# Kernel optimization log

Measured on AMD Instinct MI355X. Metric: run time of the kernel, lower is better.

## Reference

```python
import jax, jax.numpy as jnp
import numpy as np

NUM_HEADS = 16
NUM_COMPRESSED_TOKENS = 16


def _make_merge(metric, r):
    # metric: [b, t, d]; indices are computed under stop_gradient (torch no_grad)
    metric = jax.lax.stop_gradient(metric)
    metric = metric / jnp.linalg.norm(metric, axis=-1, keepdims=True)
    a, b = metric[:, ::2], metric[:, 1::2]          # [b, t/2, d] each
    scores = jnp.einsum('btd,bsd->bts', a, b)       # [b, t/2, t/2], d is small (64)
    node_max = scores.max(axis=-1)                  # [b, t/2]
    node_idx = scores.argmax(axis=-1)               # [b, t/2]
    edge_idx = jnp.argsort(-node_max, axis=-1)      # descending
    unm_idx = edge_idx[:, r:]                       # [b, t/2 - r]
    src_idx = edge_idx[:, :r]                       # [b, r]
    dst_idx = jnp.take_along_axis(node_idx, src_idx, axis=-1)  # [b, r]

    def merge(x):
        # x: [b, t, c] -> [b, t - r, c]
        src, dst = x[:, ::2], x[:, 1::2]
        bb = x.shape[0]
        unm = jnp.take_along_axis(src, unm_idx[..., None], axis=1)
        srcg = jnp.take_along_axis(src, src_idx[..., None], axis=1)
        bidx = jnp.arange(bb)[:, None]
        dst = dst.at[bidx, dst_idx].add(srcg)
        return jnp.concatenate([unm, dst], axis=1)

    return merge


def _merge_wavg(merge, x, size):
    if size is None:
        size = jnp.ones_like(x[..., :1])
    x = merge(x * size)
    size = merge(size)
    return x / size, size


def _merge_tokens(x, target_num_token):
    b, p, c = x.shape
    assert p > target_num_token
    # build merge schedule from static shapes (python ints)
    tmp_p = p
    r_merge_list = []
    while tmp_p != target_num_token:
        if tmp_p - target_num_token <= tmp_p // 2:
            r_merge_list.append(tmp_p - target_num_token)
            break
        else:
            r_merge_list.append(tmp_p // 2)
            tmp_p = tmp_p - tmp_p // 2
    dim = c // NUM_HEADS
    size = None
    for r in r_merge_list:
        p = x.shape[1]
        metric = x.reshape(b, p, NUM_HEADS, dim).mean(axis=2)  # [b, p, dim]
        merge = _make_merge(metric, r)
        x, size = _merge_wavg(merge, x, size)
    return x


def setup_inputs() -> dict:
    key = jax.random.key(0)
    k1, k2, k3 = jax.random.split(key, 3)
    vision_dim, llm_dim = 1024, 4096
    x = jax.random.normal(k1, (32, 576, vision_dim), dtype=jnp.float32)
    W1 = jax.random.normal(k2, (vision_dim, llm_dim), dtype=jnp.float32) * 0.02
    b1 = jnp.zeros((llm_dim,), dtype=jnp.float32)
    W2 = jax.random.normal(k3, (llm_dim, llm_dim), dtype=jnp.float32) * 0.02
    b2 = jnp.zeros((llm_dim,), dtype=jnp.float32)
    return {"x": x, "W1": W1, "b1": b1, "W2": W2, "b2": b2,
            "compress": 1, "local_num_frames": -1}


def reference(x, W1, b1, W2, b2, compress, local_num_frames):
    if compress:
        if local_num_frames != -1:
            num_frames = local_num_frames
            x = x.reshape(x.shape[0], -1, x.shape[-1])
        else:
            num_frames = x.shape[0]
            x = x.reshape(1, -1, x.shape[-1])
        num_tome_tokens = NUM_COMPRESSED_TOKENS * num_frames
    else:
        num_tome_tokens = NUM_COMPRESSED_TOKENS * local_num_frames
    x = _merge_tokens(x, num_tome_tokens)
    # projector: Linear -> GELU(exact) -> Linear
    h = jax.nn.gelu(jnp.einsum('btc,cd->btd', x, W1) + b1, approximate=False)
    out = jnp.einsum('btd,de->bte', h, W2) + b2
    return out
```

## Files before the change

kernel.cpp:

```cpp
#include <hip/hip_runtime.h>
#include <hip/hip_bf16.h>


typedef __attribute__((ext_vector_type(8))) short bf16x8;
typedef __attribute__((ext_vector_type(4))) float f32x4;

__global__ __launch_bounds__(256) void metric_kernel(const float* __restrict__ x,
                                                     float* __restrict__ mnorm, int p)
{
    int row  = blockIdx.x * 4 + (threadIdx.x >> 6);
    int lane = threadIdx.x & 63;
    if (row >= p) return;
    const float* xr = x + (size_t)row * 1024;
    float m = 0.f;
#pragma unroll
    for (int h = 0; h < 16; ++h) m += xr[h * 64 + lane];
    m *= 0.0625f;
    float s = m * m;
#pragma unroll
    for (int off = 32; off > 0; off >>= 1) s += __shfl_xor(s, off, 64);
    mnorm[(size_t)row * 64 + lane] = m / sqrtf(s);
}

__global__ __launch_bounds__(256) void scores_kernel(const float* __restrict__ metric,
                                                     float* __restrict__ pmax,
                                                     int* __restrict__ pidx, int P2)
{
    __shared__ float As[64 * 68];
    __shared__ float Bs[64 * 68];
    const int t = threadIdx.x;
    const int i0 = blockIdx.x * 64, j0 = blockIdx.y * 64;

#pragma unroll
    for (int u = 0; u < 16; ++u) {
        int idx = u * 256 + t;
        int d = idx & 63, i = idx >> 6;
        int gi = i0 + i;
        As[d * 68 + i] = (gi < P2) ? metric[(size_t)(2 * gi) * 64 + d] : 0.f;
        int gj = j0 + i;
        Bs[d * 68 + i] = (gj < P2) ? metric[(size_t)(2 * gj + 1) * 64 + d] : 0.f;
    }
    __syncthreads();

    const int tx = t & 15, ty = t >> 4;
    float acc[4][4];
#pragma unroll
    for (int u = 0; u < 4; ++u)
#pragma unroll
        for (int v = 0; v < 4; ++v) acc[u][v] = 0.f;

    for (int d = 0; d < 64; ++d) {
        float4 av = *reinterpret_cast<const float4*>(&As[d * 68 + ty * 4]);
        float4 bv = *reinterpret_cast<const float4*>(&Bs[d * 68 + tx * 4]);
        float a_[4] = {av.x, av.y, av.z, av.w};
        float b_[4] = {bv.x, bv.y, bv.z, bv.w};
#pragma unroll
        for (int u = 0; u < 4; ++u)
#pragma unroll
            for (int v = 0; v < 4; ++v)
                acc[u][v] = fmaf(a_[u], b_[v], acc[u][v]);
    }

#pragma unroll
    for (int u = 0; u < 4; ++u) {
        float best = -3.0e38f; int bj = 0x7fffffff;
#pragma unroll
        for (int v = 0; v < 4; ++v) {
            int j = j0 + tx * 4 + v;
            if (j < P2 && acc[u][v] > best) { best = acc[u][v]; bj = j; }
        }
#pragma unroll
        for (int off = 1; off < 16; off <<= 1) {
            float ob = __shfl_xor(best, off, 64);
            int   oj = __shfl_xor(bj,   off, 64);
            if (ob > best || (ob == best && oj < bj)) { best = ob; bj = oj; }
        }
        if (tx == 0) {
            int gi = i0 + ty * 4 + u;
            if (gi < P2) {
                pmax[(size_t)blockIdx.y * P2 + gi] = best;
                pidx[(size_t)blockIdx.y * P2 + gi] = bj;
            }
        }
    }
}

__global__ __launch_bounds__(256) void reduce_kernel(const float* __restrict__ pmax,
                                                     const int* __restrict__ pidx,
                                                     float* __restrict__ nmax,
                                                     int* __restrict__ nidx,
                                                     int P2, int JS)
{
    int i = blockIdx.x * 256 + threadIdx.x;
    if (i >= P2) return;
    float best = -3.3e38f; int bj = 0;
    for (int js = 0; js < JS; ++js) {
        float v = pmax[(size_t)js * P2 + i];
        if (v > best) { best = v; bj = pidx[(size_t)js * P2 + i]; }
    }
    nmax[i] = best; nidx[i] = bj;
}

__global__ __launch_bounds__(256) void merge_kernel(const float* __restrict__ x,
                                                    const float* __restrict__ size_in,
                                                    const int* __restrict__ nidx,
                                                    const float* __restrict__ nmax,
                                                    float* __restrict__ xout,
                                                    float* __restrict__ size_out, int P2)
{
    int j = blockIdx.x;
    __shared__ int   list[128];
    __shared__ int   cnt_s;
    __shared__ float ns_s;
    if (threadIdx.x == 0) cnt_s = 0;
    __syncthreads();
    for (int i = threadIdx.x; i < P2; i += 256) {
        if (nidx[i] == j) { int p = atomicAdd(&cnt_s, 1); if (p < 128) list[p] = i; }
    }
    __syncthreads();
    int total = cnt_s;
    bool over = (total > 128);
    if (threadIdx.x == 0) {
        float ns = size_in ? size_in[2 * j + 1] : 1.0f;
        if (!over) {
            for (int u = 1; u < total; ++u) {
                int v = list[u]; float kv = nmax[v]; int w = u - 1;
                while (w >= 0) {
                    int lw = list[w]; float kw = nmax[lw];
                    if (kw < kv || (kw == kv && lw > v)) { list[w + 1] = lw; --w; }
                    else break;
                }
                list[w + 1] = v;
            }
            for (int u = 0; u < total; ++u) ns += size_in ? size_in[2 * list[u]] : 1.0f;
        } else {
            for (int i = 0; i < P2; ++i)
                if (nidx[i] == j) ns += size_in ? size_in[2 * i] : 1.0f;
        }
        ns_s = ns;
        size_out[j] = ns;
    }
    __syncthreads();
    float ns   = ns_s;
    float sodd = size_in ? size_in[2 * j + 1] : 1.0f;
    for (int c = threadIdx.x; c < 1024; c += 256) {
        float acc = x[(size_t)(2 * j + 1) * 1024 + c] * sodd;
        if (!over) {
            for (int u = 0; u < total; ++u) {
                int i2 = list[u];
                float si = size_in ? size_in[2 * i2] : 1.0f;
                acc += x[(size_t)(2 * i2) * 1024 + c] * si;
            }
        } else {
            for (int i2 = 0; i2 < P2; ++i2) {
                if (nidx[i2] == j) {
                    float si = size_in ? size_in[2 * i2] : 1.0f;
                    acc += x[(size_t)(2 * i2) * 1024 + c] * si;
                }
            }
        }
        xout[(size_t)j * 1024 + c] = acc / ns;
    }
}

__global__ __launch_bounds__(512) void rank_kernel(const float* __restrict__ nmax,
                                                   int* __restrict__ edgeidx, int n)
{
    int i = threadIdx.x;
    if (i >= n) return;
    float v = nmax[i];
    int r = 0;
    for (int k = 0; k < n; ++k) {
        float u = nmax[k];
        if (u > v || (u == v && k < i)) ++r;
    }
    edgeidx[r] = i;
}

__global__ __launch_bounds__(256) void unm_kernel(const float* __restrict__ x,
                                                  const float* __restrict__ size_in,
                                                  const int* __restrict__ edgeidx,
                                                  float* __restrict__ xout, int r)
{
    int tb = blockIdx.x;
    int i = edgeidx[r + tb];
    float s = size_in[2 * i];
    for (int c = threadIdx.x; c < 1024; c += 256)
        xout[(size_t)tb * 1024 + c] = (x[(size_t)(2 * i) * 1024 + c] * s) / s;
}

__global__ __launch_bounds__(256) void dst6_kernel(const float* __restrict__ x,
                                                   const float* __restrict__ size_in,
                                                   const int* __restrict__ edgeidx,
                                                   const int* __restrict__ nidx,
                                                   float* __restrict__ xout,
                                                   int r, int out_off)
{
    int j = blockIdx.x;
    __shared__ int   list[64];
    __shared__ int   cnt_s;
    __shared__ float ns_s;
    if (threadIdx.x == 0) {
        int n = 0; float ns = size_in[2 * j + 1];
        for (int m = 0; m < r; ++m) {
            int i2 = edgeidx[m];
            if (nidx[i2] == j) { list[n++] = i2; ns += size_in[2 * i2]; }
        }
        cnt_s = n; ns_s = ns;
    }
    __syncthreads();
    int n = cnt_s; float ns = ns_s;
    float sodd = size_in[2 * j + 1];
    for (int c = threadIdx.x; c < 1024; c += 256) {
        float acc = x[(size_t)(2 * j + 1) * 1024 + c] * sodd;
        for (int u = 0; u < n; ++u) {
            int i2 = list[u];
            acc += x[(size_t)(2 * i2) * 1024 + c] * size_in[2 * i2];
        }
        xout[(size_t)(out_off + j) * 1024 + c] = acc / ns;
    }
}

__global__ __launch_bounds__(256) void castx_kernel(const float* __restrict__ in,
                                                    __hip_bfloat16* __restrict__ out, int n)
{
    int i = blockIdx.x * 256 + threadIdx.x;
    if (i < n) out[i] = __float2bfloat16(in[i]);
}

__global__ __launch_bounds__(256) void transcast_kernel(const float* __restrict__ in,
                                                        __hip_bfloat16* __restrict__ outT,
                                                        int K, int N)
{
    __shared__ float tile[32][33];
    int n0 = blockIdx.x * 32, k0 = blockIdx.y * 32;
    int tx = threadIdx.x & 31, ty = threadIdx.x >> 5;
#pragma unroll
    for (int u = 0; u < 4; ++u) {
        int k = k0 + ty + u * 8;
        tile[ty + u * 8][tx] = in[(size_t)k * N + n0 + tx];
    }
    __syncthreads();
#pragma unroll
    for (int u = 0; u < 4; ++u) {
        int n = n0 + ty + u * 8;
        outT[(size_t)n * K + k0 + tx] = __float2bfloat16(tile[tx][ty + u * 8]);
    }
}

template <int ACT, int OUTBF16>
__global__ __launch_bounds__(256) void mfma_gemm_kernel(
    const unsigned short* __restrict__ A,
    const unsigned short* __restrict__ Bt,
    const float* __restrict__ bias,
    void* __restrict__ Cout, int M, int N, int K)
{
    __shared__ unsigned short As[64 * 64];
    __shared__ unsigned short Bs[64 * 64];
    const int t = threadIdx.x;
    const int lane = t & 63, wave = t >> 6;
    const int wm = wave >> 1, wn = wave & 1;
    const int bi = blockIdx.y * 64, bj = blockIdx.x * 64;
    const int l15 = lane & 15, lg = lane >> 4;

    f32x4 acc[2][2];
#pragma unroll
    for (int m = 0; m < 2; ++m)
#pragma unroll
        for (int n = 0; n < 2; ++n)
#pragma unroll
            for (int r = 0; r < 4; ++r) acc[m][n][r] = 0.f;

    for (int k0 = 0; k0 < K; k0 += 64) {
        __syncthreads();
#pragma unroll
        for (int q = 0; q < 2; ++q) {
            int c = q * 256 + t;
            int row = c >> 3, cc = c & 7;
            int sc = cc ^ (row & 7);
            *reinterpret_cast<int4*>(&As[row * 64 + sc * 8]) =
                *reinterpret_cast<const int4*>(A + (size_t)(bi + row) * K + k0 + cc * 8);
            *reinterpret_cast<int4*>(&Bs[row * 64 + sc * 8]) =
                *reinterpret_cast<const int4*>(Bt + (size_t)(bj + row) * K + k0 + cc * 8);
        }
        __syncthreads();
#pragma unroll
        for (int kc = 0; kc < 2; ++kc) {
            bf16x8 af[2], bfr[2];
#pragma unroll
            for (int m = 0; m < 2; ++m) {
                int row = wm * 32 + m * 16 + l15;
                int c = kc * 4 + lg;
                int sc = c ^ (row & 7);
                af[m] = *reinterpret_cast<const bf16x8*>(&As[row * 64 + sc * 8]);
            }
#pragma unroll
            for (int n = 0; n < 2; ++n) {
                int col = wn * 32 + n * 16 + l15;
                int c = kc * 4 + lg;
                int sc = c ^ (col & 7);
                bfr[n] = *reinterpret_cast<const bf16x8*>(&Bs[col * 64 + sc * 8]);
            }
#pragma unroll
            for (int m = 0; m < 2; ++m)
#pragma unroll
                for (int n = 0; n < 2; ++n)
                    acc[m][n] = __builtin_amdgcn_mfma_f32_16x16x32_bf16(
                        af[m], bfr[n], acc[m][n], 0, 0, 0);
        }
    }

#pragma unroll
    for (int m = 0; m < 2; ++m) {
#pragma unroll
        for (int n = 0; n < 2; ++n) {
            int gcol = bj + wn * 32 + n * 16 + l15;
            float bv = bias[gcol];
#pragma unroll
            for (int r = 0; r < 4; ++r) {
                int grow = bi + wm * 32 + m * 16 + lg * 4 + r;
                float v = acc[m][n][r] + bv;
                if (ACT) v = 0.5f * v * (1.0f + erff(v * 0.70710678118654752440f));
                if (OUTBF16)
                    ((__hip_bfloat16*)Cout)[(size_t)grow * N + gcol] = __float2bfloat16(v);
                else
                    ((float*)Cout)[(size_t)grow * N + gcol] = v;
            }
        }
    }
}

extern "C" void kernel_launch(void* const* d_in, const int* in_sizes, int n_in,
                              void* d_out, int out_size, void* d_ws, size_t ws_size,
                              hipStream_t stream)
{
    const float* x_in = (const float*)d_in[0];
    const float* W1   = (const float*)d_in[1];
    const float* b1   = (const float*)d_in[2];
    const float* W2   = (const float*)d_in[3];
    const float* b2   = (const float*)d_in[4];
    float* out = (float*)d_out;

    const size_t XBYTES = (size_t)9216 * 1024 * 4;
    char* base = (char*)d_ws;
    float* xA     = (float*)base;
    float* xB     = (float*)(base + XBYTES);
    float* metric = (float*)(base + 2 * XBYTES);
    char*  tail   = base + 2 * XBYTES + (size_t)18432 * 64 * 4;
    float* sizeA  = (float*)tail;               tail += 9216 * 4;
    float* sizeB  = (float*)tail;               tail += 9216 * 4;
    float* nmax   = (float*)tail;               tail += 9216 * 4;
    int*   nidx   = (int*)tail;                 tail += 9216 * 4;
    int*   edgeidx= (int*)tail;                 tail += 2048;

    __hip_bfloat16* W2t  = (__hip_bfloat16*)xA;
    __hip_bfloat16* h_bf = (__hip_bfloat16*)((char*)xB + (2u << 20));
    __hip_bfloat16* xbf  = (__hip_bfloat16*)((char*)xB + (6u << 20));
    __hip_bfloat16* W1t  = (__hip_bfloat16*)((char*)xB + (7u << 20));

    const int pcount[6] = {18432, 9216, 4608, 2304, 1152, 576};
    float* xbufs[2] = {xA, xB};
    float* sbufs[2] = {sizeA, sizeB};

    const float* xcur = x_in;
    const float* scur = nullptr;

    for (int rd = 0; rd < 6; ++rd) {
        int p  = pcount[rd];
        int P2 = p / 2;
        float* xout = xbufs[rd & 1];
        float* sout = sbufs[rd & 1];
        float* pmax = xout;
        int*   pidx = (int*)((char*)xout + (16u << 20));

        metric_kernel<<<dim3((p + 3) / 4), dim3(256), 0, stream>>>(xcur, metric, p);

        int JB = (P2 + 63) / 64;
        scores_kernel<<<dim3(JB, JB), dim3(256), 0, stream>>>(metric, pmax, pidx, P2);
        reduce_kernel<<<dim3((P2 + 255) / 256), dim3(256), 0, stream>>>(
            pmax, pidx, nmax, nidx, P2, JB);

        if (rd < 5) {
            merge_kernel<<<dim3(P2), dim3(256), 0, stream>>>(xcur, scur, nidx, nmax,
                                                             xout, sout, P2);
        } else {
            rank_kernel<<<dim3(1), dim3(512), 0, stream>>>(nmax, edgeidx, P2);
            unm_kernel<<<dim3(P2 - 64), dim3(256), 0, stream>>>(xcur, scur, edgeidx,
                                                                xout, 64);
            dst6_kernel<<<dim3(P2), dim3(256), 0, stream>>>(xcur, scur, edgeidx, nidx,
                                                            xout, 64, P2 - 64);
        }
        xcur = xout;
        scur = sout;
    }

    castx_kernel<<<dim3((512 * 1024 + 255) / 256), dim3(256), 0, stream>>>(
        xcur, xbf, 512 * 1024);
    transcast_kernel<<<dim3(4096 / 32, 1024 / 32), dim3(256), 0, stream>>>(
        W1, W1t, 1024, 4096);
    transcast_kernel<<<dim3(4096 / 32, 4096 / 32), dim3(256), 0, stream>>>(
        W2, W2t, 4096, 4096);

    mfma_gemm_kernel<1, 1><<<dim3(4096 / 64, 512 / 64), dim3(256), 0, stream>>>(
        (const unsigned short*)xbf, (const unsigned short*)W1t, b1,
        (void*)h_bf, 512, 4096, 1024);
    mfma_gemm_kernel<0, 0><<<dim3(4096 / 64, 512 / 64), dim3(256), 0, stream>>>(
        (const unsigned short*)h_bf, (const unsigned short*)W2t, b2,
        (void*)out, 512, 4096, 4096);
}
```

Before: 885.2 us.

## Widen score tiles, batch merge destinations per block, use direct global-to-LDS loads

The scores kernel now covers 128 destination columns per block (a 4x8 register tile), which halves the number of column blocks and the partial max/argmax writes the reduce step reads back. The merge kernel handles 8 destinations per block, so each block scans nidx once for all 8 instead of once per destination. The GEMM tile load uses global_load_lds to copy straight into LDS without passing through registers. The risks are higher register pressure in the scores kernel and fewer merge blocks, which lowers parallelism; the LDS swizzle for the direct load has to produce the same layout as before.

New measurement: 957.0 us. 1.08x slower.

```diff
diff --git a/kernel.cpp b/kernel.cpp
--- a/kernel.cpp
+++ b/kernel.cpp
@@ -27,9 +27,9 @@
                                                      int* __restrict__ pidx, int P2)
 {
     __shared__ float As[64 * 68];
-    __shared__ float Bs[64 * 68];
+    __shared__ float Bs[64 * 132];
     const int t = threadIdx.x;
-    const int i0 = blockIdx.x * 64, j0 = blockIdx.y * 64;
+    const int i0 = blockIdx.x * 64, j0 = blockIdx.y * 128;
 
 #pragma unroll
     for (int u = 0; u < 16; ++u) {
@@ -37,27 +37,33 @@
         int d = idx & 63, i = idx >> 6;
         int gi = i0 + i;
         As[d * 68 + i] = (gi < P2) ? metric[(size_t)(2 * gi) * 64 + d] : 0.f;
-        int gj = j0 + i;
-        Bs[d * 68 + i] = (gj < P2) ? metric[(size_t)(2 * gj + 1) * 64 + d] : 0.f;
+    }
+#pragma unroll
+    for (int u = 0; u < 32; ++u) {
+        int idx = u * 256 + t;
+        int d = idx & 63, j = idx >> 6;
+        int gj = j0 + j;
+        Bs[d * 132 + j] = (gj < P2) ? metric[(size_t)(2 * gj + 1) * 64 + d] : 0.f;
     }
     __syncthreads();
 
     const int tx = t & 15, ty = t >> 4;
-    float acc[4][4];
+    float acc[4][8];
 #pragma unroll
     for (int u = 0; u < 4; ++u)
 #pragma unroll
-        for (int v = 0; v < 4; ++v) acc[u][v] = 0.f;
+        for (int v = 0; v < 8; ++v) acc[u][v] = 0.f;
 
     for (int d = 0; d < 64; ++d) {
         float4 av = *reinterpret_cast<const float4*>(&As[d * 68 + ty * 4]);
-        float4 bv = *reinterpret_cast<const float4*>(&Bs[d * 68 + tx * 4]);
+        float4 b0 = *reinterpret_cast<const float4*>(&Bs[d * 132 + tx * 4]);
+        float4 b1 = *reinterpret_cast<const float4*>(&Bs[d * 132 + 64 + tx * 4]);
         float a_[4] = {av.x, av.y, av.z, av.w};
-        float b_[4] = {bv.x, bv.y, bv.z, bv.w};
+        float b_[8] = {b0.x, b0.y, b0.z, b0.w, b1.x, b1.y, b1.z, b1.w};
 #pragma unroll
         for (int u = 0; u < 4; ++u)
 #pragma unroll
-            for (int v = 0; v < 4; ++v)
+            for (int v = 0; v < 8; ++v)
                 acc[u][v] = fmaf(a_[u], b_[v], acc[u][v]);
     }
 
@@ -68,6 +74,11 @@
         for (int v = 0; v < 4; ++v) {
             int j = j0 + tx * 4 + v;
             if (j < P2 && acc[u][v] > best) { best = acc[u][v]; bj = j; }
+        }
+#pragma unroll
+        for (int v = 0; v < 4; ++v) {
+            int j = j0 + 64 + tx * 4 + v;
+            if (j < P2 && acc[u][4 + v] > best) { best = acc[u][4 + v]; bj = j; }
         }
 #pragma unroll
         for (int off = 1; off < 16; off <<= 1) {
@@ -101,6 +112,7 @@
     nmax[i] = best; nidx[i] = bj;
 }
 
+#define JPB 8
 __global__ __launch_bounds__(256) void merge_kernel(const float* __restrict__ x,
                                                     const float* __restrict__ size_in,
                                                     const int* __restrict__ nidx,
@@ -108,58 +120,69 @@
                                                     float* __restrict__ xout,
                                                     float* __restrict__ size_out, int P2)
 {
-    int j = blockIdx.x;
-    __shared__ int   list[128];
-    __shared__ int   cnt_s;
-    __shared__ float ns_s;
-    if (threadIdx.x == 0) cnt_s = 0;
-    __syncthreads();
-    for (int i = threadIdx.x; i < P2; i += 256) {
-        if (nidx[i] == j) { int p = atomicAdd(&cnt_s, 1); if (p < 128) list[p] = i; }
-    }
-    __syncthreads();
-    int total = cnt_s;
-    bool over = (total > 128);
-    if (threadIdx.x == 0) {
+    int j0 = blockIdx.x * JPB;
+    __shared__ int   list[JPB][128];
+    __shared__ int   cnt[JPB];
+    __shared__ float ns_s[JPB];
+    const int t = threadIdx.x;
+    if (t < JPB) cnt[t] = 0;
+    __syncthreads();
+    for (int i = t; i < P2; i += 256) {
+        int jj = nidx[i] - j0;
+        if (jj >= 0 && jj < JPB) {
+            int p = atomicAdd(&cnt[jj], 1);
+            if (p < 128) list[jj][p] = i;
+        }
+    }
+    __syncthreads();
+    if (t < JPB) {
+        int jj = t, j = j0 + jj;
+        int total = cnt[jj];
         float ns = size_in ? size_in[2 * j + 1] : 1.0f;
-        if (!over) {
+        if (total <= 128) {
             for (int u = 1; u < total; ++u) {
-                int v = list[u]; float kv = nmax[v]; int w = u - 1;
+                int v = list[jj][u]; float kv = nmax[v]; int w = u - 1;
                 while (w >= 0) {
-                    int lw = list[w]; float kw = nmax[lw];
-                    if (kw < kv || (kw == kv && lw > v)) { list[w + 1] = lw; --w; }
+                    int lw = list[jj][w]; float kw = nmax[lw];
+                    if (kw < kv || (kw == kv && lw > v)) { list[jj][w + 1] = lw; --w; }
                     else break;
                 }
-                list[w + 1] = v;
-            }
-            for (int u = 0; u < total; ++u) ns += size_in ? size_in[2 * list[u]] : 1.0f;
+                list[jj][w + 1] = v;
+            }
+            for (int u = 0; u < total; ++u)
+                ns += size_in ? size_in[2 * list[jj][u]] : 1.0f;
         } else {
             for (int i = 0; i < P2; ++i)
                 if (nidx[i] == j) ns += size_in ? size_in[2 * i] : 1.0f;
         }
-        ns_s = ns;
+        ns_s[jj] = ns;
         size_out[j] = ns;
     }
     __syncthreads();
-    float ns   = ns_s;
-    float sodd = size_in ? size_in[2 * j + 1] : 1.0f;
-    for (int c = threadIdx.x; c < 1024; c += 256) {
-        float acc = x[(size_t)(2 * j + 1) * 1024 + c] * sodd;
-        if (!over) {
-            for (int u = 0; u < total; ++u) {
-                int i2 = list[u];
-                float si = size_in ? size_in[2 * i2] : 1.0f;
-                acc += x[(size_t)(2 * i2) * 1024 + c] * si;
-            }
-        } else {
-            for (int i2 = 0; i2 < P2; ++i2) {
-                if (nidx[i2] == j) {
+    for (int jj = 0; jj < JPB; ++jj) {
+        int j = j0 + jj;
+        int total = cnt[jj];
+        bool over = (total > 128);
+        float ns = ns_s[jj];
+        float sodd = size_in ? size_in[2 * j + 1] : 1.0f;
+        for (int c = t; c < 1024; c += 256) {
+            float acc = x[(size_t)(2 * j + 1) * 1024 + c] * sodd;
+            if (!over) {
+                for (int u = 0; u < total; ++u) {
+                    int i2 = list[jj][u];
                     float si = size_in ? size_in[2 * i2] : 1.0f;
                     acc += x[(size_t)(2 * i2) * 1024 + c] * si;
                 }
-            }
-        }
-        xout[(size_t)j * 1024 + c] = acc / ns;
+            } else {
+                for (int i2 = 0; i2 < P2; ++i2) {
+                    if (nidx[i2] == j) {
+                        float si = size_in ? size_in[2 * i2] : 1.0f;
+                        acc += x[(size_t)(2 * i2) * 1024 + c] * si;
+                    }
+                }
+            }
+            xout[(size_t)j * 1024 + c] = acc / ns;
+        }
     }
 }
 
@@ -275,13 +298,16 @@
         __syncthreads();
 #pragma unroll
         for (int q = 0; q < 2; ++q) {
-            int c = q * 256 + t;
-            int row = c >> 3, cc = c & 7;
-            int sc = cc ^ (row & 7);
-            *reinterpret_cast<int4*>(&As[row * 64 + sc * 8]) =
-                *reinterpret_cast<const int4*>(A + (size_t)(bi + row) * K + k0 + cc * 8);
-            *reinterpret_cast<int4*>(&Bs[row * 64 + sc * 8]) =
-                *reinterpret_cast<const int4*>(Bt + (size_t)(bj + row) * K + k0 + cc * 8);
+            int c   = q * 256 + wave * 64 + lane;
+            int row = c >> 3;
+            int cc  = (c & 7) ^ (row & 7);
+            int ldsbase = (q * 256 + wave * 64) * 8;
+            __builtin_amdgcn_global_load_lds(
+                (const void*)(A + (size_t)(bi + row) * K + k0 + cc * 8),
+                (void*)&As[ldsbase], 16, 0, 0);
+            __builtin_amdgcn_global_load_lds(
+                (const void*)(Bt + (size_t)(bj + row) * K + k0 + cc * 8),
+                (void*)&Bs[ldsbase], 16, 0, 0);
         }
         __syncthreads();
 #pragma unroll
@@ -375,14 +401,15 @@
 
         metric_kernel<<<dim3((p + 3) / 4), dim3(256), 0, stream>>>(xcur, metric, p);
 
-        int JB = (P2 + 63) / 64;
-        scores_kernel<<<dim3(JB, JB), dim3(256), 0, stream>>>(metric, pmax, pidx, P2);
+        int IB = (P2 + 63) / 64;
+        int JB = (P2 + 127) / 128;
+        scores_kernel<<<dim3(IB, JB), dim3(256), 0, stream>>>(metric, pmax, pidx, P2);
         reduce_kernel<<<dim3((P2 + 255) / 256), dim3(256), 0, stream>>>(
             pmax, pidx, nmax, nidx, P2, JB);
 
         if (rd < 5) {
-            merge_kernel<<<dim3(P2), dim3(256), 0, stream>>>(xcur, scur, nidx, nmax,
-                                                             xout, sout, P2);
+            merge_kernel<<<dim3(P2 / JPB), dim3(256), 0, stream>>>(
+                xcur, scur, nidx, nmax, xout, sout, P2);
         } else {
             rank_kernel<<<dim3(1), dim3(512), 0, stream>>>(nmax, edgeidx, P2);
             unm_kernel<<<dim3(P2 - 64), dim3(256), 0, stream>>>(xcur, scur, edgeidx,
```
